# Performance work log

Measured on AMD Instinct MI355X. Metric: run time of the kernel, lower is better.

Reference implementation:

```python
import jax, jax.numpy as jnp
import numpy as np

NUM_BANDS = 8
NUM_CHANNELS = 16
KC = NUM_BANDS * NUM_CHANNELS
EMA_KERNEL_LENGTH = 100
DELTA = 0.1
EPS = 1e-06
S_INIT = 0.04


def setup_inputs() -> dict:
    key = jax.random.key(0)
    kx, = jax.random.split(key, 1)
    x = jax.random.normal(kx, (32, NUM_BANDS, NUM_CHANNELS, 8192), dtype=jnp.float32)
    alpha_raw = jnp.zeros((KC,), dtype=jnp.float32)
    log_s = jnp.full((KC,), float(np.log(S_INIT / (1.0 - S_INIT))), dtype=jnp.float32)
    return {"x": x, "alpha_raw": alpha_raw, "log_s": log_s}


def _build_ema_kernel(log_s):
    # (KC, 1, L_full) causal EMA kernel, then caller slices last L taps
    Lf = EMA_KERNEL_LENGTH
    s = jax.nn.sigmoid(log_s)                      # (KC,)
    j = jnp.arange(Lf, dtype=s.dtype)              # (Lf,)
    impulse = s[:, None] * (1.0 - s[:, None]) ** j[None, :]   # (KC, Lf)
    impulse = impulse / (impulse.sum(axis=1, keepdims=True) + 1e-08)
    kernel = impulse[:, ::-1]                      # flip to causal conv kernel
    return kernel[:, None, :]                      # (KC, 1, Lf)


def reference(x, alpha_raw, log_s):
    B, K, C, T = x.shape
    x_flat = x.reshape(B, KC, T)
    alpha = jax.nn.sigmoid(alpha_raw) * 0.5        # (KC,) in (0, 0.5)
    x_mag = jnp.abs(x_flat)
    L = min(EMA_KERNEL_LENGTH, T)
    kernel = _build_ema_kernel(log_s)[:, :, -L:]   # (KC, 1, L)
    x_padded = jnp.pad(x_mag, ((0, 0), (0, 0), (L - 1, 0)))
    # depthwise causal conv: groups = KC
    M = jax.lax.conv_general_dilated(
        x_padded, kernel,
        window_strides=(1,), padding='VALID',
        feature_group_count=KC,
        dimension_numbers=('NCH', 'OIH', 'NCH'))   # (B, KC, T)
    gain = jnp.clip(M, EPS, None) ** alpha[None, :, None] + DELTA
    out_flat = x_flat / gain
    return out_flat.reshape(B, K, C, T)
```

## Files before the change

### kernel.cpp

```cpp
#include <hip/hip_runtime.h>
#include <math.h>


constexpr int T      = 8192;
constexpr int KC_    = 128;
constexpr int LEN    = 100;
constexpr int BLOCK  = 512;
constexpr int CHUNK  = 4;
constexpr int SEG    = BLOCK * CHUNK;
constexpr int NSEG   = T / SEG;
constexpr int NHALO  = LEN / CHUNK;
constexpr float EPS_   = 1e-6f;
constexpr float DELTA_ = 0.1f;
constexpr float LOG2E  = 1.4426950408889634f;

typedef float f32x4 __attribute__((ext_vector_type(4)));

__device__ __forceinline__ float fast_sigmoid(float x) {
    const float e = __builtin_amdgcn_exp2f(-x * LOG2E);
    return __builtin_amdgcn_rcpf(1.0f + e);
}

__device__ __forceinline__ float gain_div(float xv, float M, float alpha) {
    const float Mc = fmaxf(M, EPS_);
    const float g  = __builtin_amdgcn_exp2f(alpha * __builtin_amdgcn_logf(Mc)) + DELTA_;
    return xv * __builtin_amdgcn_rcpf(g);
}

__global__ __launch_bounds__(BLOCK, 8) void agc_kernel(
    const float* __restrict__ x,
    const float* __restrict__ alpha_raw,
    const float* __restrict__ log_s,
    float* __restrict__ out)
{
    __shared__ float Pe[NHALO + BLOCK];

    const int bid = blockIdx.x;
    const int row = bid >> 2;
    const int seg = bid & (NSEG - 1);
    const int g0  = seg * SEG;
    const int kc  = row & (KC_ - 1);
    const int tid = threadIdx.x;
    const float* __restrict__ xrow = x + (size_t)row * T;
    float* __restrict__ orow       = out + (size_t)row * T;

    const float s     = fast_sigmoid(log_s[kc]);
    const float alpha = 0.5f * fast_sigmoid(alpha_raw[kc]);
    const float q     = 1.0f - s;
    const float lq    = __builtin_amdgcn_logf(q);
    const float qq    = q * q;
    const float q4    = qq * qq;
    const float q8    = q4 * q4;
    const float q100  = __builtin_amdgcn_exp2f(100.0f * lq);
    const float norm  = (1.0f - q100) + 1e-8f;
    const float w0    = s / norm;
    const float c3    = w0 * q100;

    const int i4 = (g0 >> 2) + tid;

    const f32x4 v = reinterpret_cast<const f32x4*>(xrow)[i4];
    f32x4 pv = {0.0f, 0.0f, 0.0f, 0.0f};
    if (seg != 0 || tid >= NHALO)
        pv = reinterpret_cast<const f32x4*>(xrow)[i4 - NHALO];

    const float a0 = fabsf(v.x),  a1 = fabsf(v.y),  a2 = fabsf(v.z),  a3 = fabsf(v.w);
    const float b0 = fabsf(pv.x), b1 = fabsf(pv.y), b2 = fabsf(pv.z), b3 = fabsf(pv.w);

    Pe[NHALO + tid] = fmaf(q, fmaf(q, fmaf(q, a0, a1), a2), a3);
    if (tid < NHALO)
        Pe[tid] = fmaf(q, fmaf(q, fmaf(q, b0, b1), b2), b3);

    __syncthreads();

    float accE = Pe[tid];
    float accO = Pe[tid + 1];
    #pragma unroll
    for (int j = 2; j <= 24; j += 2) accE = fmaf(accE, q8, Pe[tid + j]);
    #pragma unroll
    for (int j = 3; j <= 23; j += 2) accO = fmaf(accO, q8, Pe[tid + j]);
    float M = w0 * fmaf(q4, accO, accE);

    f32x4 o;
    M = fmaf(q, M, fmaf(w0, a0, -c3 * b0));
    o.x = gain_div(v.x, M, alpha);
    M = fmaf(q, M, fmaf(w0, a1, -c3 * b1));
    o.y = gain_div(v.y, M, alpha);
    M = fmaf(q, M, fmaf(w0, a2, -c3 * b2));
    o.z = gain_div(v.z, M, alpha);
    M = fmaf(q, M, fmaf(w0, a3, -c3 * b3));
    o.w = gain_div(v.w, M, alpha);

    __builtin_nontemporal_store(o, &reinterpret_cast<f32x4*>(orow)[i4]);
}

extern "C" void kernel_launch(void* const* d_in, const int* in_sizes, int n_in,
                              void* d_out, int out_size, void* d_ws, size_t ws_size,
                              hipStream_t stream) {
    const float* x         = (const float*)d_in[0];
    const float* alpha_raw = (const float*)d_in[1];
    const float* log_s     = (const float*)d_in[2];
    float* out             = (float*)d_out;
    const int nrows = in_sizes[0] / T;
    agc_kernel<<<nrows * NSEG, BLOCK, 0, stream>>>(x, alpha_raw, log_s, out);
}
```

Measured before the change: 224.6 us.

## Process eight elements per thread with 256-thread blocks in EMA gain kernel

Each thread now handles eight consecutive samples (two float4 loads) instead of four, with blocks shrunk to 256 threads so each block still covers a 2048-sample segment. The windowed EMA prefix is rebuilt as 8-sample partial sums in shared memory, with a 12-entry halo plus a 4-element tail from the preceding samples, and a single 12-step recurrence with q^8 instead of two interleaved chains. This halves the per-element shared-memory traffic and the recurrence work, but raises register use and makes each thread's dependency chain longer.

```diff
diff --git a/kernel.cpp b/kernel.cpp
--- a/kernel.cpp
+++ b/kernel.cpp
@@ -5,11 +5,11 @@
 constexpr int T      = 8192;
 constexpr int KC_    = 128;
 constexpr int LEN    = 100;
-constexpr int BLOCK  = 512;
-constexpr int CHUNK  = 4;
+constexpr int BLOCK  = 256;
+constexpr int CHUNK  = 8;
 constexpr int SEG    = BLOCK * CHUNK;
 constexpr int NSEG   = T / SEG;
-constexpr int NHALO  = LEN / CHUNK;
+constexpr int NH8    = 12;
 constexpr float EPS_   = 1e-6f;
 constexpr float DELTA_ = 0.1f;
 constexpr float LOG2E  = 1.4426950408889634f;
@@ -27,70 +27,100 @@
     return xv * __builtin_amdgcn_rcpf(g);
 }
 
+__device__ __forceinline__ float prefix8(float q, const f32x4& u, const f32x4& w) {
+    float p = fabsf(u.x);
+    p = fmaf(q, p, fabsf(u.y));
+    p = fmaf(q, p, fabsf(u.z));
+    p = fmaf(q, p, fabsf(u.w));
+    p = fmaf(q, p, fabsf(w.x));
+    p = fmaf(q, p, fabsf(w.y));
+    p = fmaf(q, p, fabsf(w.z));
+    p = fmaf(q, p, fabsf(w.w));
+    return p;
+}
+
 __global__ __launch_bounds__(BLOCK, 8) void agc_kernel(
     const float* __restrict__ x,
     const float* __restrict__ alpha_raw,
     const float* __restrict__ log_s,
     float* __restrict__ out)
 {
-    __shared__ float Pe[NHALO + BLOCK];
+    __shared__ float Pe[NH8 + BLOCK];
 
     const int bid = blockIdx.x;
     const int row = bid >> 2;
     const int seg = bid & (NSEG - 1);
-    const int g0  = seg * SEG;
+    const int g4  = (seg * SEG) >> 2;
     const int kc  = row & (KC_ - 1);
     const int tid = threadIdx.x;
     const float* __restrict__ xrow = x + (size_t)row * T;
     float* __restrict__ orow       = out + (size_t)row * T;
+    const f32x4* __restrict__ x4   = reinterpret_cast<const f32x4*>(xrow);
+    f32x4* __restrict__ o4         = reinterpret_cast<f32x4*>(orow);
 
     const float s     = fast_sigmoid(log_s[kc]);
     const float alpha = 0.5f * fast_sigmoid(alpha_raw[kc]);
     const float q     = 1.0f - s;
     const float lq    = __builtin_amdgcn_logf(q);
-    const float qq    = q * q;
-    const float q4    = qq * qq;
+    const float q4    = (q * q) * (q * q);
     const float q8    = q4 * q4;
     const float q100  = __builtin_amdgcn_exp2f(100.0f * lq);
     const float norm  = (1.0f - q100) + 1e-8f;
     const float w0    = s / norm;
     const float c3    = w0 * q100;
 
-    const int i4 = (g0 >> 2) + tid;
+    const int i40 = g4 + 2 * tid;
 
-    const f32x4 v = reinterpret_cast<const f32x4*>(xrow)[i4];
-    f32x4 pv = {0.0f, 0.0f, 0.0f, 0.0f};
-    if (seg != 0 || tid >= NHALO)
-        pv = reinterpret_cast<const f32x4*>(xrow)[i4 - NHALO];
+    const f32x4 v0 = x4[i40];
+    const f32x4 v1 = x4[i40 + 1];
+    f32x4 p0 = {0.0f, 0.0f, 0.0f, 0.0f};
+    f32x4 p1 = {0.0f, 0.0f, 0.0f, 0.0f};
+    if (seg != 0 || tid >= 13) p0 = x4[i40 - 25];
+    if (seg != 0 || tid >= 12) p1 = x4[i40 - 24];
 
-    const float a0 = fabsf(v.x),  a1 = fabsf(v.y),  a2 = fabsf(v.z),  a3 = fabsf(v.w);
-    const float b0 = fabsf(pv.x), b1 = fabsf(pv.y), b2 = fabsf(pv.z), b3 = fabsf(pv.w);
+    if (tid < NH8) {
+        f32x4 h0 = {0.0f, 0.0f, 0.0f, 0.0f};
+        f32x4 h1 = {0.0f, 0.0f, 0.0f, 0.0f};
+        if (seg != 0) {
+            h0 = x4[g4 + 2 * (tid - NH8)];
+            h1 = x4[g4 + 2 * (tid - NH8) + 1];
+        }
+        Pe[tid] = prefix8(q, h0, h1);
+    }
 
-    Pe[NHALO + tid] = fmaf(q, fmaf(q, fmaf(q, a0, a1), a2), a3);
-    if (tid < NHALO)
-        Pe[tid] = fmaf(q, fmaf(q, fmaf(q, b0, b1), b2), b3);
+    const float a0 = fabsf(v0.x), a1 = fabsf(v0.y), a2 = fabsf(v0.z), a3 = fabsf(v0.w);
+    const float a4 = fabsf(v1.x), a5 = fabsf(v1.y), a6 = fabsf(v1.z), a7 = fabsf(v1.w);
+    const float b0 = fabsf(p0.x), b1 = fabsf(p0.y), b2 = fabsf(p0.z), b3 = fabsf(p0.w);
+    const float b4 = fabsf(p1.x), b5 = fabsf(p1.y), b6 = fabsf(p1.z), b7 = fabsf(p1.w);
+
+    {
+        float p = a0;
+        p = fmaf(q, p, a1); p = fmaf(q, p, a2); p = fmaf(q, p, a3);
+        p = fmaf(q, p, a4); p = fmaf(q, p, a5); p = fmaf(q, p, a6);
+        p = fmaf(q, p, a7);
+        Pe[NH8 + tid] = p;
+    }
 
     __syncthreads();
 
-    float accE = Pe[tid];
-    float accO = Pe[tid + 1];
+    float acc = fmaf(q, fmaf(q, fmaf(q, b0, b1), b2), b3);
     #pragma unroll
-    for (int j = 2; j <= 24; j += 2) accE = fmaf(accE, q8, Pe[tid + j]);
-    #pragma unroll
-    for (int j = 3; j <= 23; j += 2) accO = fmaf(accO, q8, Pe[tid + j]);
-    float M = w0 * fmaf(q4, accO, accE);
+    for (int j = 0; j < NH8; ++j)
+        acc = fmaf(acc, q8, Pe[tid + j]);
+    float M = w0 * acc;
 
     f32x4 o;
-    M = fmaf(q, M, fmaf(w0, a0, -c3 * b0));
-    o.x = gain_div(v.x, M, alpha);
-    M = fmaf(q, M, fmaf(w0, a1, -c3 * b1));
-    o.y = gain_div(v.y, M, alpha);
-    M = fmaf(q, M, fmaf(w0, a2, -c3 * b2));
-    o.z = gain_div(v.z, M, alpha);
-    M = fmaf(q, M, fmaf(w0, a3, -c3 * b3));
-    o.w = gain_div(v.w, M, alpha);
+    M = fmaf(q, M, fmaf(w0, a0, -c3 * b0));  o.x = gain_div(v0.x, M, alpha);
+    M = fmaf(q, M, fmaf(w0, a1, -c3 * b1));  o.y = gain_div(v0.y, M, alpha);
+    M = fmaf(q, M, fmaf(w0, a2, -c3 * b2));  o.z = gain_div(v0.z, M, alpha);
+    M = fmaf(q, M, fmaf(w0, a3, -c3 * b3));  o.w = gain_div(v0.w, M, alpha);
+    __builtin_nontemporal_store(o, &o4[i40]);
 
-    __builtin_nontemporal_store(o, &reinterpret_cast<f32x4*>(orow)[i4]);
+    M = fmaf(q, M, fmaf(w0, a4, -c3 * b4));  o.x = gain_div(v1.x, M, alpha);
+    M = fmaf(q, M, fmaf(w0, a5, -c3 * b5));  o.y = gain_div(v1.y, M, alpha);
+    M = fmaf(q, M, fmaf(w0, a6, -c3 * b6));  o.z = gain_div(v1.z, M, alpha);
+    M = fmaf(q, M, fmaf(w0, a7, -c3 * b7));  o.w = gain_div(v1.w, M, alpha);
+    __builtin_nontemporal_store(o, &o4[i40 + 1]);
 }
 
 extern "C" void kernel_launch(void* const* d_in, const int* in_sizes, int n_in,
```

Result: slower. 236.6 us (+5.3%).

## Make each wavefront own its own segment with per-wave LDS halo, dropping block barrier

Applied to the files above, without the earlier changes.

Each 64-lane wavefront now processes an independent 256-element segment of a row and keeps its own LDS slice with a 25-entry halo. The block-wide __syncthreads is replaced by a wait on LDS counters, and the block size shrinks to 256. This removes block-level barriers and loads input before computing the per-channel constants. The cost is more halo reloads, since each wave re-reads 100 prior elements instead of each 2048-element block doing so. It also relies on wavefront-synchronous LDS visibility without a barrier.

```diff
diff --git a/kernel.cpp b/kernel.cpp
--- a/kernel.cpp
+++ b/kernel.cpp
@@ -4,12 +4,12 @@
 
 constexpr int T      = 8192;
 constexpr int KC_    = 128;
-constexpr int LEN    = 100;
-constexpr int BLOCK  = 512;
+constexpr int BLOCK  = 256;
+constexpr int WPB    = BLOCK / 64;
 constexpr int CHUNK  = 4;
-constexpr int SEG    = BLOCK * CHUNK;
-constexpr int NSEG   = T / SEG;
-constexpr int NHALO  = LEN / CHUNK;
+constexpr int WELE   = 64 * CHUNK;
+constexpr int WPR    = T / WELE;
+constexpr int NHALO  = 25;
 constexpr float EPS_   = 1e-6f;
 constexpr float DELTA_ = 0.1f;
 constexpr float LOG2E  = 1.4426950408889634f;
@@ -33,64 +33,63 @@
     const float* __restrict__ log_s,
     float* __restrict__ out)
 {
-    __shared__ float Pe[NHALO + BLOCK];
+    __shared__ float Pe[WPB][92];
 
-    const int bid = blockIdx.x;
-    const int row = bid >> 2;
-    const int seg = bid & (NSEG - 1);
-    const int g0  = seg * SEG;
-    const int kc  = row & (KC_ - 1);
-    const int tid = threadIdx.x;
+    const int tid  = threadIdx.x;
+    const int lane = tid & 63;
+    const int wv   = tid >> 6;
+    const int gw   = blockIdx.x * WPB + wv;
+    const int row  = gw / WPR;
+    const int wrow = gw & (WPR - 1);
+    const int kc   = row & (KC_ - 1);
     const float* __restrict__ xrow = x + (size_t)row * T;
     float* __restrict__ orow       = out + (size_t)row * T;
+    const f32x4* __restrict__ x4   = reinterpret_cast<const f32x4*>(xrow);
+    f32x4* __restrict__ o4         = reinterpret_cast<f32x4*>(orow);
+
+    const int i4 = (wrow << 6) + lane;
+
+    const f32x4 v = x4[i4];
+    f32x4 pv = {0.0f, 0.0f, 0.0f, 0.0f};
+    if (wrow != 0 || lane >= NHALO)
+        pv = x4[i4 - NHALO];
 
     const float s     = fast_sigmoid(log_s[kc]);
     const float alpha = 0.5f * fast_sigmoid(alpha_raw[kc]);
     const float q     = 1.0f - s;
     const float lq    = __builtin_amdgcn_logf(q);
-    const float qq    = q * q;
-    const float q4    = qq * qq;
+    const float q4    = (q * q) * (q * q);
     const float q8    = q4 * q4;
     const float q100  = __builtin_amdgcn_exp2f(100.0f * lq);
     const float norm  = (1.0f - q100) + 1e-8f;
     const float w0    = s / norm;
     const float c3    = w0 * q100;
 
-    const int i4 = (g0 >> 2) + tid;
-
-    const f32x4 v = reinterpret_cast<const f32x4*>(xrow)[i4];
-    f32x4 pv = {0.0f, 0.0f, 0.0f, 0.0f};
-    if (seg != 0 || tid >= NHALO)
-        pv = reinterpret_cast<const f32x4*>(xrow)[i4 - NHALO];
-
     const float a0 = fabsf(v.x),  a1 = fabsf(v.y),  a2 = fabsf(v.z),  a3 = fabsf(v.w);
     const float b0 = fabsf(pv.x), b1 = fabsf(pv.y), b2 = fabsf(pv.z), b3 = fabsf(pv.w);
 
-    Pe[NHALO + tid] = fmaf(q, fmaf(q, fmaf(q, a0, a1), a2), a3);
-    if (tid < NHALO)
-        Pe[tid] = fmaf(q, fmaf(q, fmaf(q, b0, b1), b2), b3);
+    const float pA = fmaf(q, fmaf(q, fmaf(q, a0, a1), a2), a3);
+    const float pB = fmaf(q, fmaf(q, fmaf(q, b0, b1), b2), b3);
 
-    __syncthreads();
+    Pe[wv][NHALO + lane] = pA;
+    if (lane < NHALO) Pe[wv][lane] = pB;
 
-    float accE = Pe[tid];
-    float accO = Pe[tid + 1];
+    asm volatile("s_waitcnt lgkmcnt(0)" ::: "memory");
+
+    float accE = Pe[wv][lane];
+    float accO = Pe[wv][lane + 1];
     #pragma unroll
-    for (int j = 2; j <= 24; j += 2) accE = fmaf(accE, q8, Pe[tid + j]);
+    for (int j = 2; j <= 24; j += 2) accE = fmaf(accE, q8, Pe[wv][lane + j]);
     #pragma unroll
-    for (int j = 3; j <= 23; j += 2) accO = fmaf(accO, q8, Pe[tid + j]);
+    for (int j = 3; j <= 23; j += 2) accO = fmaf(accO, q8, Pe[wv][lane + j]);
     float M = w0 * fmaf(q4, accO, accE);
 
     f32x4 o;
-    M = fmaf(q, M, fmaf(w0, a0, -c3 * b0));
-    o.x = gain_div(v.x, M, alpha);
-    M = fmaf(q, M, fmaf(w0, a1, -c3 * b1));
-    o.y = gain_div(v.y, M, alpha);
-    M = fmaf(q, M, fmaf(w0, a2, -c3 * b2));
-    o.z = gain_div(v.z, M, alpha);
-    M = fmaf(q, M, fmaf(w0, a3, -c3 * b3));
-    o.w = gain_div(v.w, M, alpha);
-
-    __builtin_nontemporal_store(o, &reinterpret_cast<f32x4*>(orow)[i4]);
+    M = fmaf(q, M, fmaf(w0, a0, -c3 * b0));  o.x = gain_div(v.x, M, alpha);
+    M = fmaf(q, M, fmaf(w0, a1, -c3 * b1));  o.y = gain_div(v.y, M, alpha);
+    M = fmaf(q, M, fmaf(w0, a2, -c3 * b2));  o.z = gain_div(v.z, M, alpha);
+    M = fmaf(q, M, fmaf(w0, a3, -c3 * b3));  o.w = gain_div(v.w, M, alpha);
+    __builtin_nontemporal_store(o, &o4[i4]);
 }
 
 extern "C" void kernel_launch(void* const* d_in, const int* in_sizes, int n_in,
@@ -101,5 +100,6 @@
     const float* log_s     = (const float*)d_in[2];
     float* out             = (float*)d_out;
     const int nrows = in_sizes[0] / T;
-    agc_kernel<<<nrows * NSEG, BLOCK, 0, stream>>>(x, alpha_raw, log_s, out);
+    const int nblocks = nrows * (T / WELE) / WPB;
+    agc_kernel<<<nblocks, BLOCK, 0, stream>>>(x, alpha_raw, log_s, out);
 }
```

Result: no change. 227.3 us (+1.2%).
